# Performance work log

Hardware: AMD Instinct MI355X
Metric: run time of the kernel (lower is better)

## Reference

```python
import jax, jax.numpy as jnp
import numpy as np

P = 16          # patch size
D = 256         # emb dim
NH = 4          # attention heads
DH = D // NH    # head dim
GS = 4          # LE-fusion group size
EPS = 1e-5
ALPHA = 1.0
DELTA = 1.0
BETA = 1.0


def setup_inputs() -> dict:
    key = jax.random.key(0)
    ks = jax.random.split(key, 12)
    B, C, H, W = 8, 1, 256, 256
    s = 0.02
    return {
        "x": jax.random.normal(ks[0], (B, C, H, W), jnp.float32),
        # patch embed as matmul over flattened patches (equivalent to Conv2d k=s=P)
        "Wp": jax.random.normal(ks[1], (C * P * P, D), jnp.float32) * s,
        "bp": jnp.zeros((D,), jnp.float32),
        "ln_g": jnp.ones((D,), jnp.float32),
        "ln_b": jnp.zeros((D,), jnp.float32),
        "Wq": jax.random.normal(ks[2], (D, D), jnp.float32) * s,
        "bq": jnp.zeros((D,), jnp.float32),
        "Wk": jax.random.normal(ks[3], (D, D), jnp.float32) * s,
        "bk": jnp.zeros((D,), jnp.float32),
        "Wv": jax.random.normal(ks[4], (D, D), jnp.float32) * s,
        "bv": jnp.zeros((D,), jnp.float32),
        "Wo": jax.random.normal(ks[5], (D, D), jnp.float32) * s,
        "bo": jnp.zeros((D,), jnp.float32),
    }


def _forward(x, Wp, bp, ln_g, ln_b, Wq, bq, Wk, bk, Wv, bv, Wo, bo):
    B, C, H, W = x.shape
    nh, nw = H // P, W // P
    N = nh * nw
    # --- patch embed: (B,C,H,W) -> (B,N,C*P*P) @ Wp ---
    patches = x.reshape(B, C, nh, P, nw, P).transpose(0, 2, 4, 1, 3, 5)
    patches = patches.reshape(B, N, C * P * P)
    z = patches @ Wp + bp  # (B, N, D)
    # --- NF-Norm: LayerNorm then NeuroFocal scaling ---
    mu = z.mean(-1, keepdims=True)
    var = ((z - mu) ** 2).mean(-1, keepdims=True)
    zn = (z - mu) * jax.lax.rsqrt(var + EPS) * ln_g + ln_b
    mu2 = zn.mean(-1, keepdims=True)
    var2 = ((zn - mu2) ** 2).mean(-1, keepdims=True)
    nf = jnp.abs(zn - mu2).sum(-1, keepdims=True) / (jnp.sqrt(var2 + EPS) + EPS)
    z = zn * (1.0 + nf)
    # --- AG-NFA attention ---
    def split(t):  # (B,N,D) -> (B,NH,N,DH)
        return t.reshape(B, N, NH, DH).transpose(0, 2, 1, 3)
    Q = split(z @ Wq + bq)
    K = split(z @ Wk + bk)
    V = split(z @ Wv + bv)
    qk = jnp.einsum("bhnd,bhmd->bhnm", Q, K)
    logits = qk / jnp.sqrt(jnp.float32(DH))
    mu_q = Q.mean(-1, keepdims=True)
    var_q = ((Q - mu_q) ** 2).mean(-1, keepdims=True)
    sigma_q = jnp.sqrt(var_q + EPS)
    nf_q = jnp.abs(Q - mu_q).sum(-1, keepdims=True) / (sigma_q + EPS)  # (B,NH,N,1)
    # ||Q_n - K_m||^2 = |Q|^2 + |K|^2 - 2 Q.K  (avoids O(N^2*d) diff tensor)
    q2 = (Q * Q).sum(-1)  # (B,NH,N)
    k2 = (K * K).sum(-1)  # (B,NH,N)
    omega = q2[..., :, None] + k2[..., None, :] - 2.0 * qk
    omega = omega / (jnp.exp(-DELTA * nf_q) + 1.0)
    A = jax.nn.softmax(logits - ALPHA * omega, axis=-1)
    out = jnp.einsum("bhnm,bhmd->bhnd", A, V)
    out = out.transpose(0, 2, 1, 3).reshape(B, N, D)
    Y = out @ Wo + bo
    # --- LE-Fusion ---
    G = N // GS
    Yg = Y.reshape(B, G, GS, D)
    E = jnp.linalg.norm(Yg, axis=-1)  # (B,G,GS)
    lam = jax.nn.softmax(BETA * E, axis=-1)[..., None]
    return (lam * Yg).sum(axis=2)  # (B, G, D)


def reference(x, Wp, bp, ln_g, ln_b, Wq, bq, Wk, bk, Wv, bv, Wo, bo):
    return _forward(x, Wp, bp, ln_g, ln_b, Wq, bq, Wk, bk, Wv, bv, Wo, bo)
```

## Files before the change

kernel.cpp:

```cpp
#include <hip/hip_runtime.h>

#define EPSF 1e-5f
#define KSTR 68
#define PSTR 260

#define FMA4(ACC, ZS, WV) \
    ACC.x = fmaf(ZS, WV.x, ACC.x); ACC.y = fmaf(ZS, WV.y, ACC.y); \
    ACC.z = fmaf(ZS, WV.z, ACC.z); ACC.w = fmaf(ZS, WV.w, ACC.w);

__device__ __forceinline__ void pass8x8(
    const float* __restrict__ W, const float* __restrict__ zr,
    float* __restrict__ ps, int kq, int ln)
{
    const float* wr = W + kq * 8192 + 4 * ln;
    const float* zb = zr + kq * 32;
    float4 a0 = make_float4(0.f,0.f,0.f,0.f), a1 = a0, a2 = a0, a3 = a0;
    float4 a4 = a0, a5 = a0, a6 = a0, a7 = a0;
    #pragma unroll
    for (int kk = 0; kk < 32; kk += 4) {
        float4 w0 = *(const float4*)(wr + (kk + 0) * 256);
        float4 w1 = *(const float4*)(wr + (kk + 1) * 256);
        float4 w2 = *(const float4*)(wr + (kk + 2) * 256);
        float4 w3 = *(const float4*)(wr + (kk + 3) * 256);
        float4 z0 = *(const float4*)(zb + 0 * 256 + kk);
        float4 z1 = *(const float4*)(zb + 1 * 256 + kk);
        float4 z2 = *(const float4*)(zb + 2 * 256 + kk);
        float4 z3 = *(const float4*)(zb + 3 * 256 + kk);
        float4 z4 = *(const float4*)(zb + 4 * 256 + kk);
        float4 z5 = *(const float4*)(zb + 5 * 256 + kk);
        float4 z6 = *(const float4*)(zb + 6 * 256 + kk);
        float4 z7 = *(const float4*)(zb + 7 * 256 + kk);
        FMA4(a0, z0.x, w0) FMA4(a0, z0.y, w1) FMA4(a0, z0.z, w2) FMA4(a0, z0.w, w3)
        FMA4(a1, z1.x, w0) FMA4(a1, z1.y, w1) FMA4(a1, z1.z, w2) FMA4(a1, z1.w, w3)
        FMA4(a2, z2.x, w0) FMA4(a2, z2.y, w1) FMA4(a2, z2.z, w2) FMA4(a2, z2.w, w3)
        FMA4(a3, z3.x, w0) FMA4(a3, z3.y, w1) FMA4(a3, z3.z, w2) FMA4(a3, z3.w, w3)
        FMA4(a4, z4.x, w0) FMA4(a4, z4.y, w1) FMA4(a4, z4.z, w2) FMA4(a4, z4.w, w3)
        FMA4(a5, z5.x, w0) FMA4(a5, z5.y, w1) FMA4(a5, z5.z, w2) FMA4(a5, z5.w, w3)
        FMA4(a6, z6.x, w0) FMA4(a6, z6.y, w1) FMA4(a6, z6.z, w2) FMA4(a6, z6.w, w3)
        FMA4(a7, z7.x, w0) FMA4(a7, z7.y, w1) FMA4(a7, z7.z, w2) FMA4(a7, z7.w, w3)
    }
    float* pp = ps + kq * 2048 + 4 * ln;
    *(float4*)(pp + 0 * 256) = a0;
    *(float4*)(pp + 1 * 256) = a1;
    *(float4*)(pp + 2 * 256) = a2;
    *(float4*)(pp + 3 * 256) = a3;
    *(float4*)(pp + 4 * 256) = a4;
    *(float4*)(pp + 5 * 256) = a5;
    *(float4*)(pp + 6 * 256) = a6;
    *(float4*)(pp + 7 * 256) = a7;
}

__device__ __forceinline__ float4 combine8(const float* __restrict__ ps, int e)
{
    float4 a = *(const float4*)(ps + e);
    #pragma unroll
    for (int k = 1; k < 8; ++k) {
        float4 u = *(const float4*)(ps + k * 2048 + e);
        a.x += u.x; a.y += u.y; a.z += u.z; a.w += u.w;
    }
    return a;
}

__global__ __launch_bounds__(512, 2) void ka_patch_nf_qkv(
    const float* __restrict__ x,
    const float* __restrict__ Wp, const float* __restrict__ bp,
    const float* __restrict__ ln_g, const float* __restrict__ ln_b,
    const float* __restrict__ Wq, const float* __restrict__ bq,
    const float* __restrict__ Wk, const float* __restrict__ bk,
    const float* __restrict__ Wv, const float* __restrict__ bv,
    float* __restrict__ Qg, float* __restrict__ Kg, float* __restrict__ Vg)
{
    extern __shared__ float sm[];
    float* zr = sm;
    float* ps = sm + 2048;

    const int tid = threadIdx.x;
    const int kq = tid >> 6, ln = tid & 63;
    const int wave = tid >> 6, lane = tid & 63;
    const int tok0 = blockIdx.x * 8;

    #pragma unroll
    for (int i = 0; i < 4; ++i) {
        int e = tid + 512 * i;
        int t = e >> 8, dd = e & 255;
        int tk = tok0 + t, b = tk >> 8, n = tk & 255;
        int ph = n >> 4, pw = n & 15, p = dd >> 4, q = dd & 15;
        zr[t * 256 + dd] = x[b * 65536 + (ph * 16 + p) * 256 + pw * 16 + q];
    }
    __syncthreads();

    pass8x8(Wp, zr, ps, kq, ln);
    __syncthreads();
    {
        int e = tid * 4;
        float4 a = combine8(ps, e);
        float4 bb = *(const float4*)(bp + (e & 255));
        a.x += bb.x; a.y += bb.y; a.z += bb.z; a.w += bb.w;
        *(float4*)(zr + e) = a;
    }
    __syncthreads();

    {
        float g[4], bb2[4], v[4];
        #pragma unroll
        for (int c = 0; c < 4; ++c) { g[c] = ln_g[lane + 64 * c]; bb2[c] = ln_b[lane + 64 * c]; }
        float s = 0.f, ss = 0.f;
        #pragma unroll
        for (int c = 0; c < 4; ++c) { v[c] = zr[wave * 256 + lane + 64 * c]; s += v[c]; ss += v[c] * v[c]; }
        #pragma unroll
        for (int o = 32; o; o >>= 1) { s += __shfl_xor(s, o); ss += __shfl_xor(ss, o); }
        float mu  = s * (1.f / 256.f);
        float var = ss * (1.f / 256.f) - mu * mu;
        float rs  = rsqrtf(var + EPSF);
        float zn[4]; float s2 = 0.f, ss2 = 0.f;
        #pragma unroll
        for (int c = 0; c < 4; ++c) {
            zn[c] = (v[c] - mu) * rs * g[c] + bb2[c];
            s2 += zn[c]; ss2 += zn[c] * zn[c];
        }
        #pragma unroll
        for (int o = 32; o; o >>= 1) { s2 += __shfl_xor(s2, o); ss2 += __shfl_xor(ss2, o); }
        float mu2  = s2 * (1.f / 256.f);
        float var2 = ss2 * (1.f / 256.f) - mu2 * mu2;
        float as = 0.f;
        #pragma unroll
        for (int c = 0; c < 4; ++c) as += fabsf(zn[c] - mu2);
        #pragma unroll
        for (int o = 32; o; o >>= 1) as += __shfl_xor(as, o);
        float nf = as / (sqrtf(var2 + EPSF) + EPSF);
        float sc = 1.f + nf;
        #pragma unroll
        for (int c = 0; c < 4; ++c) zr[wave * 256 + lane + 64 * c] = zn[c] * sc;
    }
    __syncthreads();

    {
        int e = tid * 4, t = e >> 8, d0 = e & 255;
        int tk = tok0 + t, b = tk >> 8, n = tk & 255;
        int h = d0 >> 6, dh = d0 & 63;
        const long goff = ((long)(b * 4 + h) * 256 + n) * 64 + dh;

        pass8x8(Wq, zr, ps, kq, ln);
        __syncthreads();
        {
            float4 a = combine8(ps, e);
            float4 bb = *(const float4*)(bq + d0);
            a.x += bb.x; a.y += bb.y; a.z += bb.z; a.w += bb.w;
            *(float4*)(Qg + goff) = a;
        }
        __syncthreads();

        pass8x8(Wk, zr, ps, kq, ln);
        __syncthreads();
        {
            float4 a = combine8(ps, e);
            float4 bb = *(const float4*)(bk + d0);
            a.x += bb.x; a.y += bb.y; a.z += bb.z; a.w += bb.w;
            *(float4*)(Kg + goff) = a;
        }
        __syncthreads();

        pass8x8(Wv, zr, ps, kq, ln);
        __syncthreads();
        {
            float4 a = combine8(ps, e);
            float4 bb = *(const float4*)(bv + d0);
            a.x += bb.x; a.y += bb.y; a.z += bb.z; a.w += bb.w;
            *(float4*)(Vg + goff) = a;
        }
    }
}

__global__ __launch_bounds__(512, 2) void kb_attn(
    const float* __restrict__ Qg, const float* __restrict__ Kg,
    const float* __restrict__ Vg, float* __restrict__ Og)
{
    extern __shared__ float lds[];
    float* Kl = lds;
    float* Vl = lds + 256 * KSTR;
    float* k2 = lds + 2 * 256 * KSTR;
    float* Pl = Kl;

    const int tid = threadIdx.x;
    const int xcd = blockIdx.x & 7, slot = blockIdx.x >> 3;
    const int bh = xcd * 4 + (slot >> 3);
    const int qt = slot & 7;

    const float* Qb = Qg + (bh * 256 + qt * 32) * 64;
    const float* Kb = Kg + bh * 16384;
    const float* Vb = Vg + bh * 16384;

    const int q = tid >> 4;
    const int r = tid & 15;

    {
        const float4* Ks = (const float4*)Kb;
        const float4* Vs = (const float4*)Vb;
        #pragma unroll
        for (int i = 0; i < 8; ++i) {
            int flat = tid + 512 * i;
            int row = flat >> 4, c4 = flat & 15;
            *(float4*)(Kl + row * KSTR + c4 * 4) = Ks[flat];
            *(float4*)(Vl + row * KSTR + c4 * 4) = Vs[flat];
        }
    }
    __syncthreads();

    {
        int row = tid >> 1, half = tid & 1;
        const float* kp = Kl + row * KSTR + half * 32;
        float ssq = 0.f;
        #pragma unroll
        for (int c = 0; c < 8; ++c) {
            float4 kv = *(const float4*)(kp + 4 * c);
            ssq += kv.x*kv.x + kv.y*kv.y + kv.z*kv.z + kv.w*kv.w;
        }
        ssq += __shfl_xor(ssq, 1);
        if (half == 0) k2[row] = ssq;
    }

    float4 Qr[16];
    {
        const float4* Qp = (const float4*)(Qb + q * 64);
        #pragma unroll
        for (int c = 0; c < 16; ++c) Qr[c] = Qp[c];
    }
    float fq, gq, iq;
    {
        float s = 0.f, ss = 0.f;
        #pragma unroll
        for (int c = 0; c < 16; ++c) {
            float4 v = Qr[c];
            s  += v.x + v.y + v.z + v.w;
            ss += v.x*v.x + v.y*v.y + v.z*v.z + v.w*v.w;
        }
        float mu = s * (1.f / 64.f);
        float as = 0.f;
        #pragma unroll
        for (int c = 0; c < 16; ++c) {
            float4 v = Qr[c];
            as += fabsf(v.x - mu) + fabsf(v.y - mu)
                + fabsf(v.z - mu) + fabsf(v.w - mu);
        }
        float var = ss * (1.f / 64.f) - mu * mu;
        float sg  = sqrtf(var + EPSF);
        float nf  = as / (sg + EPSF);
        float inv = 1.f / (__expf(-nf) + 1.f);
        fq = 0.125f + 2.f * inv;
        gq = ss * inv;
        iq = inv;
    }
    __syncthreads();

    float s_[16];
    #pragma unroll
    for (int j = 0; j < 16; ++j) {
        int m = r + 16 * j;
        const float* kp = Kl + m * KSTR;
        float acc = 0.f;
        #pragma unroll
        for (int c = 0; c < 16; ++c) {
            float4 kv = *(const float4*)(kp + 4 * c);
            acc += Qr[c].x*kv.x + Qr[c].y*kv.y + Qr[c].z*kv.z + Qr[c].w*kv.w;
        }
        s_[j] = acc * fq - gq - k2[m] * iq;
    }

    float M = s_[0];
    #pragma unroll
    for (int j = 1; j < 16; ++j) M = fmaxf(M, s_[j]);
    #pragma unroll
    for (int o = 1; o < 16; o <<= 1) M = fmaxf(M, __shfl_xor(M, o));
    float L = 0.f;
    #pragma unroll
    for (int j = 0; j < 16; ++j) { s_[j] = __expf(s_[j] - M); L += s_[j]; }
    #pragma unroll
    for (int o = 1; o < 16; o <<= 1) L += __shfl_xor(L, o);
    float invL = 1.f / L;

    __syncthreads();
    #pragma unroll
    for (int j = 0; j < 16; ++j) Pl[q * PSTR + r + 16 * j] = s_[j] * invL;
    __syncthreads();

    float4 a0 = make_float4(0.f, 0.f, 0.f, 0.f);
    const float* pq = Pl + q * PSTR;
    const float* vp = Vl + 4 * r;
    #pragma unroll 8
    for (int m = 0; m < 256; ++m) {
        float pw = pq[m];
        float4 v = *(const float4*)(vp + m * KSTR);
        a0.x = fmaf(pw, v.x, a0.x); a0.y = fmaf(pw, v.y, a0.y);
        a0.z = fmaf(pw, v.z, a0.z); a0.w = fmaf(pw, v.w, a0.w);
    }
    {
        int b = bh >> 2, h = bh & 3;
        int n = qt * 32 + q;
        float* op = Og + (b * 256 + n) * 256 + h * 64 + 4 * r;
        *(float4*)op = a0;
    }
}

__global__ __launch_bounds__(512, 2) void kc_wo_le(
    const float* __restrict__ Og, const float* __restrict__ Wo,
    const float* __restrict__ bo, float* __restrict__ out)
{
    extern __shared__ float sm[];
    float* yr  = sm;
    float* ps  = sm + 2048;
    float* red = sm + 18432;

    const int tid = threadIdx.x;
    const int kq = tid >> 6, ln = tid & 63;
    const int wave = tid >> 6, lane = tid & 63;
    const int tok0 = blockIdx.x * 8;

    *(float4*)(yr + tid * 4) = *(const float4*)(Og + tok0 * 256 + tid * 4);
    __syncthreads();

    pass8x8(Wo, yr, ps, kq, ln);
    __syncthreads();
    {
        int e = tid * 4;
        float4 a = combine8(ps, e);
        float4 bb = *(const float4*)(bo + (e & 255));
        a.x += bb.x; a.y += bb.y; a.z += bb.z; a.w += bb.w;
        *(float4*)(yr + e) = a;
    }
    __syncthreads();
    {
        float ssq = 0.f;
        #pragma unroll
        for (int c = 0; c < 4; ++c) {
            float v = yr[wave * 256 + lane + 64 * c];
            ssq += v * v;
        }
        #pragma unroll
        for (int o = 32; o; o >>= 1) ssq += __shfl_xor(ssq, o);
        if (lane == 0) red[wave] = sqrtf(ssq);
    }
    __syncthreads();
    {
        int g = tid >> 8, d = tid & 255;
        float e0 = red[4 * g], e1 = red[4 * g + 1], e2 = red[4 * g + 2], e3 = red[4 * g + 3];
        float m = fmaxf(fmaxf(e0, e1), fmaxf(e2, e3));
        float x0 = __expf(e0 - m), x1 = __expf(e1 - m), x2 = __expf(e2 - m), x3 = __expf(e3 - m);
        float inv = 1.f / (x0 + x1 + x2 + x3);
        float val = (x0 * yr[(4 * g) * 256 + d] + x1 * yr[(4 * g + 1) * 256 + d]
                   + x2 * yr[(4 * g + 2) * 256 + d] + x3 * yr[(4 * g + 3) * 256 + d]) * inv;
        out[(blockIdx.x * 2 + g) * 256 + d] = val;
    }
}

extern "C" void kernel_launch(void* const* d_in, const int* in_sizes, int n_in,
                              void* d_out, int out_size, void* d_ws, size_t ws_size,
                              hipStream_t stream) {
    const float* x    = (const float*)d_in[0];
    const float* Wp   = (const float*)d_in[1];
    const float* bp   = (const float*)d_in[2];
    const float* ln_g = (const float*)d_in[3];
    const float* ln_b = (const float*)d_in[4];
    const float* Wq   = (const float*)d_in[5];
    const float* bq   = (const float*)d_in[6];
    const float* Wk   = (const float*)d_in[7];
    const float* bk   = (const float*)d_in[8];
    const float* Wv   = (const float*)d_in[9];
    const float* bv   = (const float*)d_in[10];
    const float* Wo   = (const float*)d_in[11];
    const float* bo   = (const float*)d_in[12];
    float* out = (float*)d_out;

    float* ws = (float*)d_ws;
    float* Qg = ws;
    float* Kg = ws + 524288;
    float* Vg = ws + 524288 * 2;
    float* Og = ws + 524288 * 3;

    const int ka_lds = (2048 + 16384) * 4;
    const int kb_lds = (2 * 256 * KSTR + 256) * 4;
    const int kc_lds = (2048 + 16384 + 8) * 4;
    (void)hipFuncSetAttribute((const void*)ka_patch_nf_qkv,
                              hipFuncAttributeMaxDynamicSharedMemorySize, ka_lds);
    (void)hipFuncSetAttribute((const void*)kb_attn,
                              hipFuncAttributeMaxDynamicSharedMemorySize, kb_lds);
    (void)hipFuncSetAttribute((const void*)kc_wo_le,
                              hipFuncAttributeMaxDynamicSharedMemorySize, kc_lds);

    ka_patch_nf_qkv<<<256, 512, ka_lds, stream>>>(x, Wp, bp, ln_g, ln_b,
                                                  Wq, bq, Wk, bk, Wv, bv, Qg, Kg, Vg);
    kb_attn<<<256, 512, kb_lds, stream>>>(Qg, Kg, Vg, Og);
    kc_wo_le<<<256, 512, kc_lds, stream>>>(Og, Wo, bo, out);
}
```

Baseline: 49.91 us.

## Double-buffer QKV partial sums and fuse LayerNorm into reduction to cut barriers

The patch gather now loads one float4 per thread instead of four scalar loads. Bias add, LayerNorm and NeuroFocal scaling now run directly on the combined partial-sum registers, which removes an LDS round trip and a barrier. The Q, K and V projection passes alternate between two partial-sum buffers, so the barrier between each combine and the next pass can go. The output kernel computes the row norm from registers before writing, dropping another barrier. The cost is that the first kernel's LDS roughly doubles, which can lower how many blocks fit on a CU.

```diff
diff --git a/kernel.cpp b/kernel.cpp
--- a/kernel.cpp
+++ b/kernel.cpp
@@ -71,103 +71,99 @@
     float* __restrict__ Qg, float* __restrict__ Kg, float* __restrict__ Vg)
 {
     extern __shared__ float sm[];
-    float* zr = sm;
-    float* ps = sm + 2048;
+    float* zr  = sm;
+    float* psA = sm + 2048;
+    float* psB = sm + 18432;
 
     const int tid = threadIdx.x;
     const int kq = tid >> 6, ln = tid & 63;
-    const int wave = tid >> 6, lane = tid & 63;
+    const int lane = tid & 63;
     const int tok0 = blockIdx.x * 8;
 
-    #pragma unroll
-    for (int i = 0; i < 4; ++i) {
-        int e = tid + 512 * i;
+    {
+        int e = tid * 4;
         int t = e >> 8, dd = e & 255;
         int tk = tok0 + t, b = tk >> 8, n = tk & 255;
-        int ph = n >> 4, pw = n & 15, p = dd >> 4, q = dd & 15;
-        zr[t * 256 + dd] = x[b * 65536 + (ph * 16 + p) * 256 + pw * 16 + q];
-    }
-    __syncthreads();
-
-    pass8x8(Wp, zr, ps, kq, ln);
-    __syncthreads();
+        int ph = n >> 4, pw = n & 15, p = (dd >> 4) & 15, q = dd & 15;
+        *(float4*)(zr + e) =
+            *(const float4*)(x + b * 65536 + (ph * 16 + p) * 256 + pw * 16 + q);
+    }
+    __syncthreads();
+
+    pass8x8(Wp, zr, psA, kq, ln);
+    __syncthreads();
+
     {
         int e = tid * 4;
-        float4 a = combine8(ps, e);
-        float4 bb = *(const float4*)(bp + (e & 255));
-        a.x += bb.x; a.y += bb.y; a.z += bb.z; a.w += bb.w;
-        *(float4*)(zr + e) = a;
-    }
-    __syncthreads();
-
-    {
-        float g[4], bb2[4], v[4];
-        #pragma unroll
-        for (int c = 0; c < 4; ++c) { g[c] = ln_g[lane + 64 * c]; bb2[c] = ln_b[lane + 64 * c]; }
-        float s = 0.f, ss = 0.f;
-        #pragma unroll
-        for (int c = 0; c < 4; ++c) { v[c] = zr[wave * 256 + lane + 64 * c]; s += v[c]; ss += v[c] * v[c]; }
+        float4 a = combine8(psA, e);
+        float4 bb = *(const float4*)(bp + 4 * lane);
+        a.x += bb.x; a.y += bb.y; a.z += bb.z; a.w += bb.w;
+
+        float s  = a.x + a.y + a.z + a.w;
+        float ss = a.x*a.x + a.y*a.y + a.z*a.z + a.w*a.w;
         #pragma unroll
         for (int o = 32; o; o >>= 1) { s += __shfl_xor(s, o); ss += __shfl_xor(ss, o); }
         float mu  = s * (1.f / 256.f);
         float var = ss * (1.f / 256.f) - mu * mu;
         float rs  = rsqrtf(var + EPSF);
-        float zn[4]; float s2 = 0.f, ss2 = 0.f;
-        #pragma unroll
-        for (int c = 0; c < 4; ++c) {
-            zn[c] = (v[c] - mu) * rs * g[c] + bb2[c];
-            s2 += zn[c]; ss2 += zn[c] * zn[c];
-        }
+
+        float4 g  = *(const float4*)(ln_g + 4 * lane);
+        float4 b2 = *(const float4*)(ln_b + 4 * lane);
+        float4 zn;
+        zn.x = (a.x - mu) * rs * g.x + b2.x;
+        zn.y = (a.y - mu) * rs * g.y + b2.y;
+        zn.z = (a.z - mu) * rs * g.z + b2.z;
+        zn.w = (a.w - mu) * rs * g.w + b2.w;
+
+        float s2  = zn.x + zn.y + zn.z + zn.w;
+        float ss2 = zn.x*zn.x + zn.y*zn.y + zn.z*zn.z + zn.w*zn.w;
         #pragma unroll
         for (int o = 32; o; o >>= 1) { s2 += __shfl_xor(s2, o); ss2 += __shfl_xor(ss2, o); }
         float mu2  = s2 * (1.f / 256.f);
         float var2 = ss2 * (1.f / 256.f) - mu2 * mu2;
-        float as = 0.f;
-        #pragma unroll
-        for (int c = 0; c < 4; ++c) as += fabsf(zn[c] - mu2);
+
+        float as = fabsf(zn.x - mu2) + fabsf(zn.y - mu2)
+                 + fabsf(zn.z - mu2) + fabsf(zn.w - mu2);
         #pragma unroll
         for (int o = 32; o; o >>= 1) as += __shfl_xor(as, o);
         float nf = as / (sqrtf(var2 + EPSF) + EPSF);
         float sc = 1.f + nf;
-        #pragma unroll
-        for (int c = 0; c < 4; ++c) zr[wave * 256 + lane + 64 * c] = zn[c] * sc;
-    }
-    __syncthreads();
-
-    {
-        int e = tid * 4, t = e >> 8, d0 = e & 255;
-        int tk = tok0 + t, b = tk >> 8, n = tk & 255;
-        int h = d0 >> 6, dh = d0 & 63;
-        const long goff = ((long)(b * 4 + h) * 256 + n) * 64 + dh;
-
-        pass8x8(Wq, zr, ps, kq, ln);
-        __syncthreads();
-        {
-            float4 a = combine8(ps, e);
-            float4 bb = *(const float4*)(bq + d0);
-            a.x += bb.x; a.y += bb.y; a.z += bb.z; a.w += bb.w;
-            *(float4*)(Qg + goff) = a;
-        }
-        __syncthreads();
-
-        pass8x8(Wk, zr, ps, kq, ln);
-        __syncthreads();
-        {
-            float4 a = combine8(ps, e);
-            float4 bb = *(const float4*)(bk + d0);
-            a.x += bb.x; a.y += bb.y; a.z += bb.z; a.w += bb.w;
-            *(float4*)(Kg + goff) = a;
-        }
-        __syncthreads();
-
-        pass8x8(Wv, zr, ps, kq, ln);
-        __syncthreads();
-        {
-            float4 a = combine8(ps, e);
-            float4 bb = *(const float4*)(bv + d0);
-            a.x += bb.x; a.y += bb.y; a.z += bb.z; a.w += bb.w;
-            *(float4*)(Vg + goff) = a;
-        }
+        zn.x *= sc; zn.y *= sc; zn.z *= sc; zn.w *= sc;
+        *(float4*)(zr + e) = zn;
+    }
+    __syncthreads();
+
+    int e = tid * 4, t = e >> 8, d0 = e & 255;
+    int tk = tok0 + t, b = tk >> 8, n = tk & 255;
+    int h = d0 >> 6, dh = d0 & 63;
+    const long goff = ((long)(b * 4 + h) * 256 + n) * 64 + dh;
+
+    pass8x8(Wq, zr, psB, kq, ln);
+    __syncthreads();
+
+    {
+        float4 a = combine8(psB, e);
+        float4 bb = *(const float4*)(bq + d0);
+        a.x += bb.x; a.y += bb.y; a.z += bb.z; a.w += bb.w;
+        *(float4*)(Qg + goff) = a;
+    }
+    pass8x8(Wk, zr, psA, kq, ln);
+    __syncthreads();
+
+    {
+        float4 a = combine8(psA, e);
+        float4 bb = *(const float4*)(bk + d0);
+        a.x += bb.x; a.y += bb.y; a.z += bb.z; a.w += bb.w;
+        *(float4*)(Kg + goff) = a;
+    }
+    pass8x8(Wv, zr, psB, kq, ln);
+    __syncthreads();
+
+    {
+        float4 a = combine8(psB, e);
+        float4 bb = *(const float4*)(bv + d0);
+        a.x += bb.x; a.y += bb.y; a.z += bb.z; a.w += bb.w;
+        *(float4*)(Vg + goff) = a;
     }
 }
 
@@ -320,26 +316,20 @@
 
     pass8x8(Wo, yr, ps, kq, ln);
     __syncthreads();
+
     {
         int e = tid * 4;
         float4 a = combine8(ps, e);
-        float4 bb = *(const float4*)(bo + (e & 255));
-        a.x += bb.x; a.y += bb.y; a.z += bb.z; a.w += bb.w;
-        *(float4*)(yr + e) = a;
-    }
-    __syncthreads();
-    {
-        float ssq = 0.f;
-        #pragma unroll
-        for (int c = 0; c < 4; ++c) {
-            float v = yr[wave * 256 + lane + 64 * c];
-            ssq += v * v;
-        }
+        float4 bb = *(const float4*)(bo + 4 * lane);
+        a.x += bb.x; a.y += bb.y; a.z += bb.z; a.w += bb.w;
+        float ssq = a.x*a.x + a.y*a.y + a.z*a.z + a.w*a.w;
         #pragma unroll
         for (int o = 32; o; o >>= 1) ssq += __shfl_xor(ssq, o);
         if (lane == 0) red[wave] = sqrtf(ssq);
-    }
-    __syncthreads();
+        *(float4*)(yr + e) = a;
+    }
+    __syncthreads();
+
     {
         int g = tid >> 8, d = tid & 255;
         float e0 = red[4 * g], e1 = red[4 * g + 1], e2 = red[4 * g + 2], e3 = red[4 * g + 3];
@@ -376,7 +366,7 @@
     float* Vg = ws + 524288 * 2;
     float* Og = ws + 524288 * 3;
 
-    const int ka_lds = (2048 + 16384) * 4;
+    const int ka_lds = (2048 + 2 * 16384) * 4;
     const int kb_lds = (2 * 256 * KSTR + 256) * 4;
     const int kc_lds = (2048 + 16384 + 8) * 4;
     (void)hipFuncSetAttribute((const void*)ka_patch_nf_qkv,
```

New measurement: 49.73 us (median of 3 runs). No clear change (-0.4%).
